# Kernel tuning notes

Measured on AMD Instinct MI355X. Metric: run time of the kernel, lower is better.

## Reference

```python
import jax, jax.numpy as jnp
import numpy as np

NUM_CODES = 1024
CODE_DIM = 256
SPLITS = 2
EMA_DECAY = 0.99
COMMITMENT = 0.25
EPS = 1e-6


def setup_inputs() -> dict:
    key = jax.random.key(0)
    k1, k2, k3 = jax.random.split(key, 3)
    z = jax.random.normal(k1, (32, 512, 1, SPLITS * CODE_DIM), dtype=jnp.float32)
    embedding = jax.random.normal(k2, (NUM_CODES, CODE_DIM), dtype=jnp.float32)
    cluster_size = jnp.zeros((NUM_CODES,), dtype=jnp.float32)
    embedding_avg = jax.random.normal(k3, (NUM_CODES, CODE_DIM), dtype=jnp.float32)
    return {"z": z, "embedding": embedding, "cluster_size": cluster_size,
            "embedding_avg": embedding_avg}


def reference(z, embedding, cluster_size, embedding_avg):
    orig_shape = z.shape
    # split last dim into (SPLITS, CODE_DIM); all splits share the codebook
    zs = z.reshape(*orig_shape[:-1], SPLITS, CODE_DIM)
    flat = zs.reshape(-1, CODE_DIM)                       # [N, D]
    dist = (jnp.sum(flat * flat, axis=1, keepdims=True)
            - 2.0 * flat @ embedding.T
            + jnp.sum(embedding * embedding, axis=1))      # [N, K]
    indices = jnp.argmin(dist, axis=1)                     # [N]
    z_q = embedding[indices].reshape(zs.shape)

    # EMA statistics (training-mode buffer updates), scatter-based histogram
    counts = jnp.zeros((NUM_CODES,), dtype=flat.dtype).at[indices].add(1.0)
    embed_sum = jnp.zeros((NUM_CODES, CODE_DIM), dtype=flat.dtype).at[indices].add(flat)
    new_cluster_size = EMA_DECAY * cluster_size + (1.0 - EMA_DECAY) * counts
    new_embedding_avg = EMA_DECAY * embedding_avg + (1.0 - EMA_DECAY) * embed_sum
    n = jnp.sum(new_cluster_size)
    cs = (new_cluster_size + EPS) / (n + NUM_CODES * EPS) * n
    cs = jnp.maximum(cs, EPS)
    embed_normalized = new_embedding_avg / cs[:, None]     # dead-code random
    # resurrection (data-dependent randint) intentionally omitted

    loss = COMMITMENT * jnp.mean((jax.lax.stop_gradient(z_q) - zs) ** 2)
    z_q_st = zs + jax.lax.stop_gradient(z_q - zs)          # straight-through
    z_q_flat = z_q_st.reshape(orig_shape)
    idx_out = indices.reshape(*orig_shape[:-1], SPLITS)
    return (z_q_flat, loss, idx_out, new_cluster_size, new_embedding_avg,
            embed_normalized)
```

## Files before the change

### kernel.cpp

```cpp
#include <hip/hip_runtime.h>

#define NUM_CODES 1024
#define CODE_DIM  256
#define N_ROWS    32768

#define ZQ_OFF    0
#define LOSS_OFF  8388608
#define IDX_OFF   8388609
#define CS_OFF    8421377
#define NEA_OFF   8422401
#define NORM_OFF  8684545
#define ZERO_CNT  295937

#define EMA       0.99f
#define ONE_M_EMA 0.01f
#define EPSF      1e-6f

#define WS_N      0
#define WS_ENORM  16
#define WS_EH_B   8192
#define WS_EL_B   (8192 + 524288)

typedef __attribute__((ext_vector_type(8))) short short8;
typedef __attribute__((ext_vector_type(4))) float f32x4;

__device__ __forceinline__ unsigned short f2bf(float x) {
  union { float f; unsigned u; } v; v.f = x;
  unsigned r = v.u + 0x7fffu + ((v.u >> 16) & 1u);
  return (unsigned short)(r >> 16);
}
__device__ __forceinline__ float bf2f(unsigned short b) {
  union { unsigned u; float f; } v; v.u = ((unsigned)b) << 16;
  return v.f;
}

typedef const __attribute__((address_space(1))) unsigned char* gas_t;
typedef __attribute__((address_space(3))) unsigned char* las_t;
__device__ __forceinline__ void gl_lds16(const void* g, void* l) {
  __builtin_amdgcn_global_load_lds((gas_t)g, (las_t)l, 16, 0, 0);
}

__global__ void k_setup(const float* __restrict__ emb, float* __restrict__ out,
                        float* __restrict__ wsf) {
  const int b = blockIdx.x, t = threadIdx.x;
  long zi = (long)b * 256 + t;
  if (zi < ZERO_CNT) out[LOSS_OFF + zi] = 0.0f;
  if (b < NUM_CODES) {
    char* wsb = (char*)wsf;
    float x = emb[(long)b * CODE_DIM + t];
    unsigned short hb = f2bf(x);
    unsigned short lb = f2bf(x - bf2f(hb));
    unsigned short* eh = (unsigned short*)(wsb + WS_EH_B);
    unsigned short* el = (unsigned short*)(wsb + WS_EL_B);
    int p = t >> 3, j = t & 7;
    long eo = ((long)p * NUM_CODES + b) * 8 + j;
    eh[eo] = hb; el[eo] = lb;
    float v = x * x;
    #pragma unroll
    for (int o = 32; o >= 1; o >>= 1) v += __shfl_xor(v, o);
    __shared__ float s[4];
    if ((t & 63) == 0) s[t >> 6] = v;
    __syncthreads();
    if (t == 0) wsf[WS_ENORM + b] = s[0] + s[1] + s[2] + s[3];
  }
}

#define BM        64
#define NC        32
#define NCHUNK    32
#define CHUNK_B   32768

__launch_bounds__(256, 2)
__global__ void k_main(const float* __restrict__ z, const float* __restrict__ emb,
                       const float* __restrict__ wsf, float* __restrict__ out) {
  __shared__ __align__(16) unsigned char lds[2 * CHUNK_B];
  __shared__ int   s_idx[BM];
  __shared__ float s_l[4];

  const char* wsb = (const char*)wsf;
  const int tid = threadIdx.x;
  const int w   = tid >> 6;
  const int l   = tid & 63;
  const int mrow = l & 15;
  const int kq   = l >> 4;
  const int row0 = blockIdx.x * BM;
  const long arow = row0 + w * 16 + mrow;

  short8 aH[8], aL[8];
  const float* zr = z + arow * CODE_DIM + kq * 8;
  #pragma unroll
  for (int ks = 0; ks < 8; ++ks) {
    float4 f0 = *(const float4*)(zr + ks * 32);
    float4 f1 = *(const float4*)(zr + ks * 32 + 4);
    float xs[8] = {f0.x, f0.y, f0.z, f0.w, f1.x, f1.y, f1.z, f1.w};
    #pragma unroll
    for (int j = 0; j < 8; ++j) {
      unsigned short hb = f2bf(xs[j]);
      aH[ks][j] = (short)hb;
      aL[ks][j] = (short)f2bf(xs[j] - bf2f(hb));
    }
  }

  auto stage = [&](int chunk, int buf) {
    #pragma unroll
    for (int it = 0; it < 8; ++it) {
      int d  = (it * 256 + tid) * 16;
      int s  = d >> 14;
      int d2 = d & 16383;
      int p  = d2 >> 9;
      int in_ = d2 & 511;
      const char* src = wsb + (s ? WS_EL_B : WS_EH_B) + p * 16384 + chunk * 512 + in_;
      gl_lds16(src, (void*)(lds + buf * CHUNK_B + d));
    }
  };

  float best[4]; int bidx[4];
  #pragma unroll
  for (int r = 0; r < 4; ++r) { best[r] = 3.0e38f; bidx[r] = 0; }

  stage(0, 0);
  for (int c = 0; c < NCHUNK; ++c) {
    __syncthreads();
    if (c + 1 < NCHUNK) stage(c + 1, (c + 1) & 1);
    const unsigned char* base = lds + (c & 1) * CHUNK_B;
    #pragma unroll
    for (int nt = 0; nt < 2; ++nt) {
      f32x4 accA = {0.f, 0.f, 0.f, 0.f};
      f32x4 accB = {0.f, 0.f, 0.f, 0.f};
      f32x4 accC = {0.f, 0.f, 0.f, 0.f};
      const int ci = nt * 16 + mrow;
      #pragma unroll
      for (int ks = 0; ks < 8; ++ks) {
        const int p = ks * 4 + kq;
        short8 bh = *(const short8*)(base + (p * NC + ci) * 16);
        short8 bl = *(const short8*)(base + 16384 + (p * NC + ci) * 16);
        accA = __builtin_amdgcn_mfma_f32_16x16x32_bf16(aH[ks], bh, accA, 0, 0, 0);
        accB = __builtin_amdgcn_mfma_f32_16x16x32_bf16(aL[ks], bh, accB, 0, 0, 0);
        accC = __builtin_amdgcn_mfma_f32_16x16x32_bf16(aH[ks], bl, accC, 0, 0, 0);
      }
      const int code = c * NC + nt * 16 + mrow;
      const float en = wsf[WS_ENORM + code];
      #pragma unroll
      for (int r = 0; r < 4; ++r) {
        float dot = accA[r] + accB[r] + accC[r];
        float sv = fmaf(-2.0f, dot, en);
        if (sv < best[r]) { best[r] = sv; bidx[r] = code; }
      }
    }
  }

  #pragma unroll
  for (int r = 0; r < 4; ++r) {
    float v = best[r]; int ix = bidx[r];
    #pragma unroll
    for (int o = 1; o < 16; o <<= 1) {
      float v2 = __shfl_xor(v, o);
      int   x2 = __shfl_xor(ix, o);
      if (v2 < v || (v2 == v && x2 < ix)) { v = v2; ix = x2; }
    }
    if (mrow == 0) s_idx[w * 16 + kq * 4 + r] = ix;
  }
  __syncthreads();

  if (tid < BM) {
    int ix = s_idx[tid];
    out[IDX_OFF + row0 + tid] = (float)ix;
    atomicAdd(&out[CS_OFF + ix], 1.0f);
  }

  float lacc = 0.0f;
  for (int r = 0; r < BM; ++r) {
    int ix = s_idx[r];
    long zo = (long)(row0 + r) * CODE_DIM + tid;
    float ev = emb[(long)ix * CODE_DIM + tid];
    float xv = z[zo];
    float df = ev - xv;
    out[ZQ_OFF + zo] = xv + df;
    lacc += df * df;
    atomicAdd(&out[NEA_OFF + (long)ix * CODE_DIM + tid], xv);
  }
  #pragma unroll
  for (int o = 32; o >= 1; o >>= 1) lacc += __shfl_xor(lacc, o);
  if (l == 0) s_l[w] = lacc;
  __syncthreads();
  if (tid == 0) {
    float t = 0.f;
    #pragma unroll
    for (int k = 0; k < 4; ++k) t += s_l[k];
    atomicAdd(&out[LOSS_OFF], t);
  }
}

__global__ void k_fin1(const float* __restrict__ cs_in, float* __restrict__ out,
                       float* __restrict__ wsf) {
  const int t = threadIdx.x;
  float counts = out[CS_OFF + t];
  float ncs = EMA * cs_in[t] + ONE_M_EMA * counts;
  out[CS_OFF + t] = ncs;
  float v = ncs;
  #pragma unroll
  for (int o = 32; o >= 1; o >>= 1) v += __shfl_xor(v, o);
  __shared__ float s[16];
  if ((t & 63) == 0) s[t >> 6] = v;
  __syncthreads();
  if (t == 0) {
    float n = 0.0f;
    #pragma unroll
    for (int k = 0; k < 16; ++k) n += s[k];
    wsf[WS_N] = n;
  }
}

__global__ void k_fin2(const float* __restrict__ ea, float* __restrict__ out,
                       const float* __restrict__ wsf) {
  const int k = blockIdx.x, d = threadIdx.x;
  __shared__ float s_cs;
  if (d == 0) {
    float n   = wsf[WS_N];
    float ncs = out[CS_OFF + k];
    float cs  = (ncs + EPSF) / (n + (float)NUM_CODES * EPSF) * n;
    s_cs = fmaxf(cs, EPSF);
  }
  __syncthreads();
  long o = (long)k * CODE_DIM + d;
  float esum = out[NEA_OFF + o];
  float nea  = EMA * ea[o] + ONE_M_EMA * esum;
  out[NEA_OFF + o] = nea;
  out[NORM_OFF + o] = nea / s_cs;
  if (k == 0 && d == 0) out[LOSS_OFF] *= (0.25f / 8388608.0f);
}

extern "C" void kernel_launch(void* const* d_in, const int* in_sizes, int n_in,
                              void* d_out, int out_size, void* d_ws, size_t ws_size,
                              hipStream_t stream) {
  const float* z   = (const float*)d_in[0];
  const float* emb = (const float*)d_in[1];
  const float* cs  = (const float*)d_in[2];
  const float* ea  = (const float*)d_in[3];
  float* out = (float*)d_out;
  float* wsf = (float*)d_ws;

  hipLaunchKernelGGL(k_setup, dim3(1157), dim3(256), 0, stream, emb, out, wsf);
  hipLaunchKernelGGL(k_main,  dim3(N_ROWS / BM), dim3(256), 0, stream, z, emb, wsf, out);
  hipLaunchKernelGGL(k_fin1,  dim3(1), dim3(1024), 0, stream, cs, out, wsf);
  hipLaunchKernelGGL(k_fin2,  dim3(NUM_CODES), dim3(CODE_DIM), 0, stream, ea, out, wsf);
}
```

Baseline: 146.1 us.

## Replace float atomics in EMA sums with counting-sort gather per code

The argmin kernel now only writes indices and integer counts. A scan kernel computes per-code offsets, a scatter kernel builds row lists grouped by code, and a gather kernel per code produces z_q, loss, embed_sum, the EMA update and the normalised embedding without per-element float atomics. The main kernel also shrinks to 2 waves, each handling 32 rows, which gives more B-fragment reuse per LDS load. Costs are two extra launches, a serial 1024-thread scan, and load imbalance in the gather when a few codes receive many rows.

```diff
diff --git a/kernel.cpp b/kernel.cpp
--- a/kernel.cpp
+++ b/kernel.cpp
@@ -10,16 +10,21 @@
 #define CS_OFF    8421377
 #define NEA_OFF   8422401
 #define NORM_OFF  8684545
-#define ZERO_CNT  295937
 
 #define EMA       0.99f
 #define ONE_M_EMA 0.01f
 #define EPSF      1e-6f
-
-#define WS_N      0
-#define WS_ENORM  16
-#define WS_EH_B   8192
-#define WS_EL_B   (8192 + 524288)
+#define LOSS_SCALE (0.25f / 8388608.0f)
+
+#define WS_N_B      0
+#define WS_ENORM_B  64
+#define WS_CNT_B    (WS_ENORM_B + 4096)
+#define WS_OFF_B    (WS_CNT_B + 4096)
+#define WS_CUR_B    (WS_OFF_B + 4096)
+#define WS_IDX_B    (WS_CUR_B + 4096)
+#define WS_LIST_B   (WS_IDX_B + 131072)
+#define WS_EH_B     (WS_LIST_B + 131072)
+#define WS_EL_B     (WS_EH_B + 524288)
 
 typedef __attribute__((ext_vector_type(8))) short short8;
 typedef __attribute__((ext_vector_type(4))) float f32x4;
@@ -43,26 +48,26 @@
 __global__ void k_setup(const float* __restrict__ emb, float* __restrict__ out,
                         float* __restrict__ wsf) {
   const int b = blockIdx.x, t = threadIdx.x;
-  long zi = (long)b * 256 + t;
-  if (zi < ZERO_CNT) out[LOSS_OFF + zi] = 0.0f;
-  if (b < NUM_CODES) {
-    char* wsb = (char*)wsf;
-    float x = emb[(long)b * CODE_DIM + t];
-    unsigned short hb = f2bf(x);
-    unsigned short lb = f2bf(x - bf2f(hb));
-    unsigned short* eh = (unsigned short*)(wsb + WS_EH_B);
-    unsigned short* el = (unsigned short*)(wsb + WS_EL_B);
-    int p = t >> 3, j = t & 7;
-    long eo = ((long)p * NUM_CODES + b) * 8 + j;
-    eh[eo] = hb; el[eo] = lb;
-    float v = x * x;
-    #pragma unroll
-    for (int o = 32; o >= 1; o >>= 1) v += __shfl_xor(v, o);
-    __shared__ float s[4];
-    if ((t & 63) == 0) s[t >> 6] = v;
-    __syncthreads();
-    if (t == 0) wsf[WS_ENORM + b] = s[0] + s[1] + s[2] + s[3];
-  }
+  char* wsb = (char*)wsf;
+  if (b < 4) {
+    ((unsigned*)(wsb + WS_CNT_B))[b * 256 + t] = 0u;
+    if (b == 0 && t == 0) out[LOSS_OFF] = 0.0f;
+  }
+  float x = emb[(long)b * CODE_DIM + t];
+  unsigned short hb = f2bf(x);
+  unsigned short lb = f2bf(x - bf2f(hb));
+  unsigned short* eh = (unsigned short*)(wsb + WS_EH_B);
+  unsigned short* el = (unsigned short*)(wsb + WS_EL_B);
+  int p = t >> 3, j = t & 7;
+  long eo = ((long)p * NUM_CODES + b) * 8 + j;
+  eh[eo] = hb; el[eo] = lb;
+  float v = x * x;
+  #pragma unroll
+  for (int o = 32; o >= 1; o >>= 1) v += __shfl_xor(v, o);
+  __shared__ float s[4];
+  if ((t & 63) == 0) s[t >> 6] = v;
+  __syncthreads();
+  if (t == 0) ((float*)(wsb + WS_ENORM_B))[b] = s[0] + s[1] + s[2] + s[3];
 }
 
 #define BM        64
@@ -70,41 +75,47 @@
 #define NCHUNK    32
 #define CHUNK_B   32768
 
-__launch_bounds__(256, 2)
-__global__ void k_main(const float* __restrict__ z, const float* __restrict__ emb,
-                       const float* __restrict__ wsf, float* __restrict__ out) {
+__launch_bounds__(128, 1)
+__global__ void k_main(const float* __restrict__ z, const float* __restrict__ wsf,
+                       float* __restrict__ out) {
   __shared__ __align__(16) unsigned char lds[2 * CHUNK_B];
-  __shared__ int   s_idx[BM];
-  __shared__ float s_l[4];
+  __shared__ int s_idx[BM];
 
   const char* wsb = (const char*)wsf;
+  const float* enp = (const float*)(wsb + WS_ENORM_B);
   const int tid = threadIdx.x;
   const int w   = tid >> 6;
   const int l   = tid & 63;
   const int mrow = l & 15;
   const int kq   = l >> 4;
   const int row0 = blockIdx.x * BM;
-  const long arow = row0 + w * 16 + mrow;
-
-  short8 aH[8], aL[8];
-  const float* zr = z + arow * CODE_DIM + kq * 8;
-  #pragma unroll
-  for (int ks = 0; ks < 8; ++ks) {
-    float4 f0 = *(const float4*)(zr + ks * 32);
-    float4 f1 = *(const float4*)(zr + ks * 32 + 4);
-    float xs[8] = {f0.x, f0.y, f0.z, f0.w, f1.x, f1.y, f1.z, f1.w};
-    #pragma unroll
-    for (int j = 0; j < 8; ++j) {
-      unsigned short hb = f2bf(xs[j]);
-      aH[ks][j] = (short)hb;
-      aL[ks][j] = (short)f2bf(xs[j] - bf2f(hb));
+
+  short8 aH0[8], aL0[8], aH1[8], aL1[8];
+  {
+    const float* zr0 = z + (long)(row0 + w * 32 + mrow) * CODE_DIM + kq * 8;
+    const float* zr1 = zr0 + 16 * CODE_DIM;
+    #pragma unroll
+    for (int ks = 0; ks < 8; ++ks) {
+      float4 f0 = *(const float4*)(zr0 + ks * 32);
+      float4 f1 = *(const float4*)(zr0 + ks * 32 + 4);
+      float4 g0 = *(const float4*)(zr1 + ks * 32);
+      float4 g1 = *(const float4*)(zr1 + ks * 32 + 4);
+      float xs[8] = {f0.x, f0.y, f0.z, f0.w, f1.x, f1.y, f1.z, f1.w};
+      float ys[8] = {g0.x, g0.y, g0.z, g0.w, g1.x, g1.y, g1.z, g1.w};
+      #pragma unroll
+      for (int j = 0; j < 8; ++j) {
+        unsigned short hb = f2bf(xs[j]);
+        aH0[ks][j] = (short)hb; aL0[ks][j] = (short)f2bf(xs[j] - bf2f(hb));
+        unsigned short hc = f2bf(ys[j]);
+        aH1[ks][j] = (short)hc; aL1[ks][j] = (short)f2bf(ys[j] - bf2f(hc));
+      }
     }
   }
 
   auto stage = [&](int chunk, int buf) {
     #pragma unroll
-    for (int it = 0; it < 8; ++it) {
-      int d  = (it * 256 + tid) * 16;
+    for (int it = 0; it < 16; ++it) {
+      int d  = (it * 128 + tid) * 16;
       int s  = d >> 14;
       int d2 = d & 16383;
       int p  = d2 >> 9;
@@ -114,9 +125,11 @@
     }
   };
 
-  float best[4]; int bidx[4];
-  #pragma unroll
-  for (int r = 0; r < 4; ++r) { best[r] = 3.0e38f; bidx[r] = 0; }
+  float best0[4], best1[4]; int bidx0[4], bidx1[4];
+  #pragma unroll
+  for (int r = 0; r < 4; ++r) {
+    best0[r] = 3.0e38f; bidx0[r] = 0; best1[r] = 3.0e38f; bidx1[r] = 0;
+  }
 
   stage(0, 0);
   for (int c = 0; c < NCHUNK; ++c) {
@@ -125,109 +138,147 @@
     const unsigned char* base = lds + (c & 1) * CHUNK_B;
     #pragma unroll
     for (int nt = 0; nt < 2; ++nt) {
-      f32x4 accA = {0.f, 0.f, 0.f, 0.f};
-      f32x4 accB = {0.f, 0.f, 0.f, 0.f};
-      f32x4 accC = {0.f, 0.f, 0.f, 0.f};
+      f32x4 aA0 = {0,0,0,0}, aB0 = {0,0,0,0}, aC0 = {0,0,0,0};
+      f32x4 aA1 = {0,0,0,0}, aB1 = {0,0,0,0}, aC1 = {0,0,0,0};
       const int ci = nt * 16 + mrow;
       #pragma unroll
       for (int ks = 0; ks < 8; ++ks) {
         const int p = ks * 4 + kq;
         short8 bh = *(const short8*)(base + (p * NC + ci) * 16);
         short8 bl = *(const short8*)(base + 16384 + (p * NC + ci) * 16);
-        accA = __builtin_amdgcn_mfma_f32_16x16x32_bf16(aH[ks], bh, accA, 0, 0, 0);
-        accB = __builtin_amdgcn_mfma_f32_16x16x32_bf16(aL[ks], bh, accB, 0, 0, 0);
-        accC = __builtin_amdgcn_mfma_f32_16x16x32_bf16(aH[ks], bl, accC, 0, 0, 0);
+        aA0 = __builtin_amdgcn_mfma_f32_16x16x32_bf16(aH0[ks], bh, aA0, 0, 0, 0);
+        aA1 = __builtin_amdgcn_mfma_f32_16x16x32_bf16(aH1[ks], bh, aA1, 0, 0, 0);
+        aB0 = __builtin_amdgcn_mfma_f32_16x16x32_bf16(aL0[ks], bh, aB0, 0, 0, 0);
+        aB1 = __builtin_amdgcn_mfma_f32_16x16x32_bf16(aL1[ks], bh, aB1, 0, 0, 0);
+        aC0 = __builtin_amdgcn_mfma_f32_16x16x32_bf16(aH0[ks], bl, aC0, 0, 0, 0);
+        aC1 = __builtin_amdgcn_mfma_f32_16x16x32_bf16(aH1[ks], bl, aC1, 0, 0, 0);
       }
       const int code = c * NC + nt * 16 + mrow;
-      const float en = wsf[WS_ENORM + code];
+      const float en = enp[code];
       #pragma unroll
       for (int r = 0; r < 4; ++r) {
-        float dot = accA[r] + accB[r] + accC[r];
-        float sv = fmaf(-2.0f, dot, en);
-        if (sv < best[r]) { best[r] = sv; bidx[r] = code; }
+        float d0 = aA0[r] + aB0[r] + aC0[r];
+        float s0 = fmaf(-2.0f, d0, en);
+        if (s0 < best0[r]) { best0[r] = s0; bidx0[r] = code; }
+        float d1 = aA1[r] + aB1[r] + aC1[r];
+        float s1 = fmaf(-2.0f, d1, en);
+        if (s1 < best1[r]) { best1[r] = s1; bidx1[r] = code; }
       }
     }
   }
 
   #pragma unroll
   for (int r = 0; r < 4; ++r) {
-    float v = best[r]; int ix = bidx[r];
+    float v = best0[r]; int ix = bidx0[r];
     #pragma unroll
     for (int o = 1; o < 16; o <<= 1) {
-      float v2 = __shfl_xor(v, o);
-      int   x2 = __shfl_xor(ix, o);
+      float v2 = __shfl_xor(v, o); int x2 = __shfl_xor(ix, o);
       if (v2 < v || (v2 == v && x2 < ix)) { v = v2; ix = x2; }
     }
-    if (mrow == 0) s_idx[w * 16 + kq * 4 + r] = ix;
+    if (mrow == 0) s_idx[w * 32 + kq * 4 + r] = ix;
+    float u = best1[r]; int iy = bidx1[r];
+    #pragma unroll
+    for (int o = 1; o < 16; o <<= 1) {
+      float u2 = __shfl_xor(u, o); int y2 = __shfl_xor(iy, o);
+      if (u2 < u || (u2 == u && y2 < iy)) { u = u2; iy = y2; }
+    }
+    if (mrow == 0) s_idx[w * 32 + 16 + kq * 4 + r] = iy;
   }
   __syncthreads();
 
   if (tid < BM) {
     int ix = s_idx[tid];
     out[IDX_OFF + row0 + tid] = (float)ix;
-    atomicAdd(&out[CS_OFF + ix], 1.0f);
-  }
-
-  float lacc = 0.0f;
-  for (int r = 0; r < BM; ++r) {
-    int ix = s_idx[r];
-    long zo = (long)(row0 + r) * CODE_DIM + tid;
-    float ev = emb[(long)ix * CODE_DIM + tid];
-    float xv = z[zo];
-    float df = ev - xv;
-    out[ZQ_OFF + zo] = xv + df;
-    lacc += df * df;
-    atomicAdd(&out[NEA_OFF + (long)ix * CODE_DIM + tid], xv);
-  }
-  #pragma unroll
-  for (int o = 32; o >= 1; o >>= 1) lacc += __shfl_xor(lacc, o);
-  if (l == 0) s_l[w] = lacc;
-  __syncthreads();
-  if (tid == 0) {
-    float t = 0.f;
-    #pragma unroll
-    for (int k = 0; k < 4; ++k) t += s_l[k];
-    atomicAdd(&out[LOSS_OFF], t);
-  }
-}
-
-__global__ void k_fin1(const float* __restrict__ cs_in, float* __restrict__ out,
+    ((unsigned*)((char*)wsf + WS_IDX_B))[row0 + tid] = (unsigned)ix;
+    atomicAdd(&((unsigned*)((char*)wsf + WS_CNT_B))[ix], 1u);
+  }
+}
+
+__global__ void k_scan(const float* __restrict__ cs_in, float* __restrict__ out,
                        float* __restrict__ wsf) {
+  __shared__ unsigned ps[NUM_CODES];
+  __shared__ float ns[16];
+  char* wsb = (char*)wsf;
   const int t = threadIdx.x;
-  float counts = out[CS_OFF + t];
-  float ncs = EMA * cs_in[t] + ONE_M_EMA * counts;
+  unsigned cnt = ((unsigned*)(wsb + WS_CNT_B))[t];
+  float ncs = EMA * cs_in[t] + ONE_M_EMA * (float)cnt;
   out[CS_OFF + t] = ncs;
   float v = ncs;
   #pragma unroll
   for (int o = 32; o >= 1; o >>= 1) v += __shfl_xor(v, o);
-  __shared__ float s[16];
-  if ((t & 63) == 0) s[t >> 6] = v;
-  __syncthreads();
+  if ((t & 63) == 0) ns[t >> 6] = v;
+  ps[t] = cnt;
+  __syncthreads();
+  #pragma unroll
+  for (int o = 1; o < NUM_CODES; o <<= 1) {
+    unsigned add = (t >= o) ? ps[t - o] : 0u;
+    __syncthreads();
+    ps[t] += add;
+    __syncthreads();
+  }
+  unsigned excl = ps[t] - cnt;
+  ((unsigned*)(wsb + WS_OFF_B))[t] = excl;
+  ((unsigned*)(wsb + WS_CUR_B))[t] = excl;
   if (t == 0) {
     float n = 0.0f;
     #pragma unroll
-    for (int k = 0; k < 16; ++k) n += s[k];
-    wsf[WS_N] = n;
-  }
-}
-
-__global__ void k_fin2(const float* __restrict__ ea, float* __restrict__ out,
-                       const float* __restrict__ wsf) {
-  const int k = blockIdx.x, d = threadIdx.x;
-  __shared__ float s_cs;
-  if (d == 0) {
-    float n   = wsf[WS_N];
-    float ncs = out[CS_OFF + k];
-    float cs  = (ncs + EPSF) / (n + (float)NUM_CODES * EPSF) * n;
-    s_cs = fmaxf(cs, EPSF);
-  }
-  __syncthreads();
-  long o = (long)k * CODE_DIM + d;
-  float esum = out[NEA_OFF + o];
-  float nea  = EMA * ea[o] + ONE_M_EMA * esum;
+    for (int k = 0; k < 16; ++k) n += ns[k];
+    *((float*)(wsb + WS_N_B)) = n;
+  }
+}
+
+__global__ void k_scatter(float* __restrict__ wsf) {
+  char* wsb = (char*)wsf;
+  int r = blockIdx.x * 256 + threadIdx.x;
+  unsigned ix = ((unsigned*)(wsb + WS_IDX_B))[r];
+  unsigned slot = atomicAdd(&((unsigned*)(wsb + WS_CUR_B))[ix], 1u);
+  ((unsigned*)(wsb + WS_LIST_B))[slot] = r;
+}
+
+__global__ void k_gather(const float* __restrict__ z, const float* __restrict__ emb,
+                         const float* __restrict__ ea, float* __restrict__ out,
+                         const float* __restrict__ wsf) {
+  __shared__ unsigned slist[4096];
+  __shared__ float sl[4];
+  const char* wsb = (const char*)wsf;
+  const int k = blockIdx.x, t = threadIdx.x;
+  const unsigned cnt = ((const unsigned*)(wsb + WS_CNT_B))[k];
+  const unsigned off = ((const unsigned*)(wsb + WS_OFF_B))[k];
+  const unsigned* list = (const unsigned*)(wsb + WS_LIST_B);
+
+  const float e = emb[(long)k * CODE_DIM + t];
+  float sum = 0.0f, lacc = 0.0f;
+
+  for (unsigned base = 0; base < cnt; base += 4096) {
+    unsigned m = cnt - base; if (m > 4096) m = 4096;
+    for (unsigned i = t; i < m; i += 256) slist[i] = list[off + base + i];
+    __syncthreads();
+    for (unsigned i = 0; i < m; ++i) {
+      long zo = (long)slist[i] * CODE_DIM + t;
+      float x = z[zo];
+      float d = e - x;
+      out[ZQ_OFF + zo] = x + d;
+      lacc += d * d;
+      sum += x;
+    }
+    __syncthreads();
+  }
+
+  long o = (long)k * CODE_DIM + t;
+  float nea = EMA * ea[o] + ONE_M_EMA * sum;
   out[NEA_OFF + o] = nea;
-  out[NORM_OFF + o] = nea / s_cs;
-  if (k == 0 && d == 0) out[LOSS_OFF] *= (0.25f / 8388608.0f);
+  float n   = *((const float*)(wsb + WS_N_B));
+  float ncs = out[CS_OFF + k];
+  float cs  = (ncs + EPSF) / (n + (float)NUM_CODES * EPSF) * n;
+  cs = fmaxf(cs, EPSF);
+  out[NORM_OFF + o] = nea / cs;
+
+  #pragma unroll
+  for (int ofs = 32; ofs >= 1; ofs >>= 1) lacc += __shfl_xor(lacc, ofs);
+  if ((t & 63) == 0) sl[t >> 6] = lacc;
+  __syncthreads();
+  if (t == 0)
+    atomicAdd(&out[LOSS_OFF], (sl[0] + sl[1] + sl[2] + sl[3]) * LOSS_SCALE);
 }
 
 extern "C" void kernel_launch(void* const* d_in, const int* in_sizes, int n_in,
@@ -240,8 +291,9 @@
   float* out = (float*)d_out;
   float* wsf = (float*)d_ws;
 
-  hipLaunchKernelGGL(k_setup, dim3(1157), dim3(256), 0, stream, emb, out, wsf);
-  hipLaunchKernelGGL(k_main,  dim3(N_ROWS / BM), dim3(256), 0, stream, z, emb, wsf, out);
-  hipLaunchKernelGGL(k_fin1,  dim3(1), dim3(1024), 0, stream, cs, out, wsf);
-  hipLaunchKernelGGL(k_fin2,  dim3(NUM_CODES), dim3(CODE_DIM), 0, stream, ea, out, wsf);
-}
+  hipLaunchKernelGGL(k_setup,   dim3(NUM_CODES), dim3(256), 0, stream, emb, out, wsf);
+  hipLaunchKernelGGL(k_main,    dim3(N_ROWS / BM), dim3(128), 0, stream, z, wsf, out);
+  hipLaunchKernelGGL(k_scan,    dim3(1), dim3(1024), 0, stream, cs, out, wsf);
+  hipLaunchKernelGGL(k_scatter, dim3(N_ROWS / 256), dim3(256), 0, stream, wsf);
+  hipLaunchKernelGGL(k_gather,  dim3(NUM_CODES), dim3(256), 0, stream, z, emb, ea, out, wsf);
+}
```

After: 196.8 us. 1.35x slower.
